# Performance work log

Measured on AMD Instinct MI355X. Metric: run time of the kernel, lower is better.

## Reference

```python
import jax, jax.numpy as jnp
import numpy as np

IOU_THR = 0.5
NEG_POS = 3
CONF_W = 1.0
LOC_W = 1.0


def setup_inputs() -> dict:
    key = jax.random.key(0)
    ks = jax.random.split(key, 6)
    B, A, G = 16, 65536, 32
    ac = jax.random.uniform(ks[0], (B, A, 2))
    asz = jax.random.uniform(ks[1], (B, A, 2)) * 0.28 + 0.02
    anchors = jnp.concatenate([ac - asz / 2, ac + asz / 2], -1)
    gc = jax.random.uniform(ks[2], (B, G, 2))
    gsz = jax.random.uniform(ks[3], (B, G, 2)) * 0.28 + 0.02
    gt_boxes = jnp.concatenate([gc - gsz / 2, gc + gsz / 2], -1)
    bbox_pred = anchors + 0.05 * jax.random.normal(ks[4], (B, A, 4))
    # probabilities strictly inside (0,1) for BCE
    conf_pred = jax.random.uniform(ks[5], (B, A)) * 0.98 + 0.01
    return {"bbox_pred": bbox_pred, "conf_pred": conf_pred,
            "anchors": anchors, "gt_boxes": gt_boxes}


def _box_iou(a, g):
    # a: [A,4] xyxy, g: [G,4] xyxy -> [A,G]
    lt = jnp.maximum(a[:, None, :2], g[None, :, :2])
    rb = jnp.minimum(a[:, None, 2:], g[None, :, 2:])
    wh = jnp.clip(rb - lt, 0.0)
    inter = wh[..., 0] * wh[..., 1]
    area_a = (a[:, 2] - a[:, 0]) * (a[:, 3] - a[:, 1])
    area_g = (g[:, 2] - g[:, 0]) * (g[:, 3] - g[:, 1])
    return inter / (area_a[:, None] + area_g[None, :] - inter)


def _bce(p, t):
    return -(t * jnp.log(p) + (1.0 - t) * jnp.log1p(-p))


def _smooth_l1(x):
    ax = jnp.abs(x)
    return jnp.where(ax < 1.0, 0.5 * ax * ax, ax - 0.5)


def _per_image(bp, cp, an, gt):
    # bp: [A,4] pred boxes, cp: [A] conf, an: [A,4] anchors, gt: [G,4]
    A = cp.shape[0]
    ious = _box_iou(an, gt)                      # [A,G]
    best_gt_iou = ious.max(1)                    # [A]
    best_gt_idx = ious.argmax(1)                 # [A]
    best_anchor_idx = ious.argmax(0)             # [G] force-match each gt
    mask = (best_gt_iou > IOU_THR).at[best_anchor_idx].set(True)
    num_pos = mask.sum()

    # localization loss (center/size parameterization), summed over positives
    matched = gt[best_gt_idx]                    # [A,4]
    pc = (bp[:, :2] + bp[:, 2:]) / 2
    ps = bp[:, 2:] - bp[:, :2]
    gc = (matched[:, :2] + matched[:, 2:]) / 2
    gs = matched[:, 2:] - matched[:, :2]
    loc = _smooth_l1(jnp.concatenate([pc, ps], 1) - jnp.concatenate([gc, gs], 1)).sum(1)
    loc_loss = jnp.where(mask, loc, 0.0).sum()

    # confidence loss with hard negative mining
    t = mask.astype(cp.dtype)
    bce = _bce(cp, t)
    pos_loss = jnp.where(mask, bce, 0.0).sum()
    neg_bce = jnp.where(mask, 0.0, bce)
    num_neg = jnp.minimum(num_pos * NEG_POS, A - num_pos)
    sorted_neg = -jnp.sort(-neg_bce)             # descending
    neg_loss = jnp.where(jnp.arange(A) < num_neg, sorted_neg, 0.0).sum()
    conf_loss = pos_loss / jnp.maximum(num_pos, 1) + neg_loss / jnp.maximum(num_neg, 1)
    return loc_loss, conf_loss, num_pos


def reference(bbox_pred, conf_pred, anchors, gt_boxes):
    loc, conf, npos = jax.vmap(_per_image)(bbox_pred, conf_pred, anchors, gt_boxes)
    B = bbox_pred.shape[0]
    total_npos = jnp.maximum(npos.sum(), 1)
    total_loc = loc.sum() / total_npos * LOC_W
    total_conf = conf.sum() / B * CONF_W
    return total_loc + total_conf
```

## Files before the change

### kernel.cpp

```cpp
#include <hip/hip_runtime.h>

#define BB 16
#define AA 65536
#define GG 32
#define NB 8192
#define KOFF 59904u
#define MBLK (AA / 256)
#define NSEG 16
#define SEGA (AA / NSEG)

__device__ unsigned char      g_mask[(size_t)BB * AA];
__device__ unsigned char      g_bidx[(size_t)BB * AA];
__device__ unsigned long long g_fpart[(size_t)BB * GG * MBLK];
__device__ unsigned int       g_hpart[(size_t)BB * NSEG * (NB/2)];
__device__ float g_spart[BB * NSEG * 2];
__device__ int   g_npart[BB * NSEG];
__device__ float g_loc[BB], g_pos[BB], g_neg[BB];
__device__ int   g_npos[BB], g_nneg[BB];

__device__ __forceinline__ float iou_f(float ax0, float ay0, float ax1, float ay1,
                                       float gx0, float gy0, float gx1, float gy1) {
    float lx = fmaxf(ax0, gx0), ly = fmaxf(ay0, gy0);
    float rx = fminf(ax1, gx1), ry = fminf(ay1, gy1);
    float w = fmaxf(rx - lx, 0.0f), h = fmaxf(ry - ly, 0.0f);
    float inter = w * h;
    float areaa = (ax1 - ax0) * (ay1 - ay0);
    float areag = (gx1 - gx0) * (gy1 - gy0);
    return inter / (areaa + areag - inter);
}

__device__ __forceinline__ float midval(int bin) {
    return __uint_as_float((((unsigned int)bin + KOFF) << 14) | 8192u);
}

__global__ void k_matchforce(const float4* __restrict__ anchors,
                             const float4* __restrict__ gts) {
    __shared__ float4 sg[GG];
    __shared__ unsigned long long wkey[4][GG];
    const int b = blockIdx.y;
    const int t = threadIdx.x;
    if (t < GG) sg[t] = gts[(size_t)b * GG + t];
    __syncthreads();
    const int a = blockIdx.x * 256 + t;
    const int wave = t >> 6, lane = t & 63;
    const float4 av = anchors[(size_t)b * AA + a];
    float best = -1.0f;
    int bg = 0;
#pragma unroll
    for (int g = 0; g < GG; ++g) {
        const float4 gb = sg[g];
        const float v = iou_f(av.x, av.y, av.z, av.w, gb.x, gb.y, gb.z, gb.w);
        if (v > best) { best = v; bg = g; }
        float m = v;
#pragma unroll
        for (int off = 1; off < 64; off <<= 1) m = fmaxf(m, __shfl_xor(m, off, 64));
        const unsigned long long bal = __ballot(v == m);
        const int first = __ffsll((unsigned long long)bal) - 1;
        if (lane == 0) {
            const unsigned int wa = (unsigned int)(blockIdx.x * 256 + wave * 64 + first);
            wkey[wave][g] = ((unsigned long long)__float_as_uint(m) << 32) |
                            (unsigned long long)(0xFFFFFFFFu - wa);
        }
    }
    g_mask[(size_t)b * AA + a] = (best > 0.5f) ? 1 : 0;
    g_bidx[(size_t)b * AA + a] = (unsigned char)bg;
    __syncthreads();
    if (t < GG) {
        unsigned long long k0 = wkey[0][t];
#pragma unroll
        for (int w = 1; w < 4; ++w) { unsigned long long k1 = wkey[w][t]; if (k1 > k0) k0 = k1; }
        g_fpart[((size_t)b * GG + t) * MBLK + blockIdx.x] = k0;
    }
}

__global__ void k_redforce() {
    const int g = blockIdx.x, b = blockIdx.y, t = threadIdx.x;
    __shared__ unsigned long long red[256];
    red[t] = g_fpart[((size_t)b * GG + g) * MBLK + t];
    __syncthreads();
    for (int w = 128; w > 0; w >>= 1) {
        if (t < w) { if (red[t + w] > red[t]) red[t] = red[t + w]; }
        __syncthreads();
    }
    if (t == 0) {
        const unsigned int a = 0xFFFFFFFFu - (unsigned int)(red[0] & 0xFFFFFFFFull);
        g_mask[(size_t)b * AA + a] = 1;
    }
}

__global__ void k_stats(const float4* __restrict__ bbox,
                        const float* __restrict__ conf,
                        const float4* __restrict__ gts) {
    __shared__ float4 sg[GG];
    __shared__ unsigned int hp[NB / 2];
    __shared__ float rf[256], rf2[256];
    __shared__ unsigned int ru[256];
    const int b = blockIdx.y, seg = blockIdx.x, t = threadIdx.x;
    if (t < GG) sg[t] = gts[(size_t)b * GG + t];
    for (int j = t; j < NB / 2; j += 256) hp[j] = 0u;
    __syncthreads();

    const size_t base = (size_t)b * AA + (size_t)seg * SEGA;
    const float4* c4 = (const float4*)(conf + base);
    const uchar4* m4 = (const uchar4*)(g_mask + base);
    const uchar4* x4 = (const uchar4*)(g_bidx + base);
    const float4* bb4 = bbox + base;

    float pos = 0.0f, loc = 0.0f;
    int np = 0;
#pragma unroll
    for (int j = 0; j < SEGA / 1024; ++j) {
        const int idx = j * 256 + t;
        const float4 p4 = c4[idx];
        const uchar4 mm = m4[idx];
        const uchar4 xx = x4[idx];
        const float pv[4] = {p4.x, p4.y, p4.z, p4.w};
        const unsigned char mv[4] = {mm.x, mm.y, mm.z, mm.w};
        const unsigned char xv[4] = {xx.x, xx.y, xx.z, xx.w};
#pragma unroll
        for (int c = 0; c < 4; ++c) {
            const float p = pv[c];
            if (mv[c]) {
                np += 1;
                pos += -logf(p);
                const float4 bv = bb4[4 * idx + c];
                const float4 gb = sg[xv[c]];
                const float d0 = (bv.x + bv.z) * 0.5f - (gb.x + gb.z) * 0.5f;
                const float d1 = (bv.y + bv.w) * 0.5f - (gb.y + gb.w) * 0.5f;
                const float d2 = (bv.z - bv.x) - (gb.z - gb.x);
                const float d3 = (bv.w - bv.y) - (gb.w - gb.y);
                float ds[4] = {d0, d1, d2, d3};
#pragma unroll
                for (int q = 0; q < 4; ++q) {
                    float ax = fabsf(ds[q]);
                    loc += (ax < 1.0f) ? 0.5f * ax * ax : ax - 0.5f;
                }
            } else {
                const float nb = -log1pf(-p);
                int key = (int)(__float_as_uint(nb) >> 14) - (int)KOFF;
                key = key < 0 ? 0 : (key > NB - 1 ? NB - 1 : key);
                atomicAdd(&hp[key >> 1], 1u << ((key & 1) << 4));
            }
        }
    }
    ru[t] = (unsigned int)np; rf[t] = pos; rf2[t] = loc;
    __syncthreads();
    for (int w = 128; w > 0; w >>= 1) {
        if (t < w) { ru[t] += ru[t + w]; rf[t] += rf[t + w]; rf2[t] += rf2[t + w]; }
        __syncthreads();
    }
    if (t == 0) {
        g_npart[b * NSEG + seg] = (int)ru[0];
        g_spart[(b * NSEG + seg) * 2 + 0] = rf[0];
        g_spart[(b * NSEG + seg) * 2 + 1] = rf2[0];
    }
    unsigned int* outp = g_hpart + ((size_t)b * NSEG + seg) * (NB / 2);
    for (int j = t; j < NB / 2; j += 256) outp[j] = hp[j];
}

__global__ void __launch_bounds__(1024) k_select() {
    __shared__ unsigned int hist[NB];
    __shared__ unsigned int ru[1024];
    __shared__ unsigned int s2[32];
    __shared__ float sh_pos, sh_loc;
    __shared__ int sh_np, sh_k, sh_bsel;
    __shared__ unsigned int sh_take;
    __shared__ float rf[1024];

    const int b = blockIdx.x, t = threadIdx.x;
    for (int w = t; w < NB / 2; w += 1024) {
        unsigned int lo = 0, hi = 0;
#pragma unroll
        for (int s = 0; s < NSEG; ++s) {
            const unsigned int v = g_hpart[((size_t)b * NSEG + s) * (NB / 2) + w];
            lo += v & 0xFFFFu; hi += v >> 16;
        }
        hist[2 * w] = lo; hist[2 * w + 1] = hi;
    }
    if (t == 0) {
        int np = 0; float pos = 0.0f, loc = 0.0f;
        for (int s = 0; s < NSEG; ++s) {
            np += g_npart[b * NSEG + s];
            pos += g_spart[(b * NSEG + s) * 2 + 0];
            loc += g_spart[(b * NSEG + s) * 2 + 1];
        }
        sh_np = np; sh_pos = pos; sh_loc = loc;
    }
    __syncthreads();
    const int np_tot = sh_np;

    unsigned int c = 0;
    const int hi = NB - 1 - t * 8;
#pragma unroll
    for (int j = 0; j < 8; ++j) c += hist[hi - j];
    ru[t] = c;
    __syncthreads();
    if (t < 32) {
        unsigned int x = 0;
#pragma unroll
        for (int j = 0; j < 32; ++j) x += ru[t * 32 + j];
        s2[t] = x;
    }
    __syncthreads();
    if (t == 0) {
        int k = 3 * np_tot;
        const int maxneg = AA - np_tot;
        if (k > maxneg) k = maxneg;
        sh_k = k;
        int bsel = NB;
        unsigned int take = 0;
        if (k > 0) {
            unsigned int cum = 0;
            int u = 0;
            while (u < 31 && cum + s2[u] < (unsigned int)k) { cum += s2[u]; ++u; }
            int cc = u * 32;
            while (cc < 1023 && cum + ru[cc] < (unsigned int)k) { cum += ru[cc]; ++cc; }
            const int h2 = NB - 1 - cc * 8;
            int j = 0;
            while (j < 7 && cum + hist[h2 - j] < (unsigned int)k) { cum += hist[h2 - j]; ++j; }
            bsel = h2 - j;
            take = (unsigned int)k - cum;
        }
        sh_bsel = bsel; sh_take = take;
    }
    __syncthreads();
    const int bsel = sh_bsel;
    float negp = 0.0f;
    for (int j = t; j < NB; j += 1024)
        if (j > bsel) { unsigned int cnt = hist[j]; if (cnt) negp += (float)cnt * midval(j); }
    rf[t] = negp;
    __syncthreads();
    for (int w = 512; w > 0; w >>= 1) {
        if (t < w) rf[t] += rf[t + w];
        __syncthreads();
    }
    if (t == 0) {
        float neg = 0.0f;
        if (sh_k > 0) neg = rf[0] + (float)sh_take * midval(bsel < NB ? bsel : 0);
        g_loc[b] = sh_loc; g_pos[b] = sh_pos; g_neg[b] = neg;
        g_npos[b] = np_tot; g_nneg[b] = sh_k;
    }
}

__global__ void k_final(unsigned int* __restrict__ out) {
    if (threadIdx.x == 0) {
        float loc = 0.0f, conf = 0.0f;
        int tot = 0;
        for (int b = 0; b < BB; ++b) {
            loc += g_loc[b];
            const int np = g_npos[b], nn = g_nneg[b];
            conf += g_pos[b] / (float)(np > 1 ? np : 1) +
                    g_neg[b] / (float)(nn > 1 ? nn : 1);
            tot += np;
        }
        const float total = loc / (float)(tot > 1 ? tot : 1) + conf / (float)BB;
        unsigned int u = __float_as_uint(total);
        unsigned int r = 0x7FFFu + ((u >> 16) & 1u);
        unsigned int bf = (u + r) >> 16;
        out[0] = (bf << 16) | bf;
    }
}

extern "C" void kernel_launch(void* const* d_in, const int* in_sizes, int n_in,
                              void* d_out, int out_size, void* d_ws, size_t ws_size,
                              hipStream_t stream) {
    const float4* bbox    = (const float4*)d_in[0];
    const float*  conf    = (const float*)d_in[1];
    const float4* anchors = (const float4*)d_in[2];
    const float4* gts     = (const float4*)d_in[3];

    k_matchforce<<<dim3(MBLK, BB), 256, 0, stream>>>(anchors, gts);
    k_redforce<<<dim3(GG, BB), 256, 0, stream>>>();
    k_stats<<<dim3(NSEG, BB), 256, 0, stream>>>(bbox, conf, gts);
    k_select<<<BB, 1024, 0, stream>>>();
    k_final<<<1, 64, 0, stream>>>((unsigned int*)d_out);
}
```

Measured before the change: 153.9 us.

## Restructure anchor-GT matching: multi-anchor per thread, ratio metric, LDS atomic argmax

Each thread now handles four anchors and keeps a per-GT running best in registers, replacing the per-GT wave shuffle reduction with shared-memory atomicMax/atomicMin over value and index. IoU is replaced by inter/(areaA+areaG), using a fast reciprocal, and the threshold becomes 1/3, which is equivalent to IoU > 0.5. The second-stage reduction shrinks to one 64-lane wave shuffle because there are fewer partial blocks. This aims to cut shuffle and division cost in the matching kernel, at the cost of more registers and approximate reciprocal precision that may change tie-breaking or argmax choices.

Result: no change. 153.1 us (-0.5%).

```diff
diff --git a/kernel.cpp b/kernel.cpp
--- a/kernel.cpp
+++ b/kernel.cpp
@@ -5,7 +5,9 @@
 #define GG 32
 #define NB 8192
 #define KOFF 59904u
-#define MBLK (AA / 256)
+#define AT 4
+#define APB (256 * AT)
+#define MBLK (AA / APB)
 #define NSEG 16
 #define SEGA (AA / NSEG)
 
@@ -18,72 +20,96 @@
 __device__ float g_loc[BB], g_pos[BB], g_neg[BB];
 __device__ int   g_npos[BB], g_nneg[BB];
 
-__device__ __forceinline__ float iou_f(float ax0, float ay0, float ax1, float ay1,
-                                       float gx0, float gy0, float gx1, float gy1) {
-    float lx = fmaxf(ax0, gx0), ly = fmaxf(ay0, gy0);
-    float rx = fminf(ax1, gx1), ry = fminf(ay1, gy1);
-    float w = fmaxf(rx - lx, 0.0f), h = fmaxf(ry - ly, 0.0f);
-    float inter = w * h;
-    float areaa = (ax1 - ax0) * (ay1 - ay0);
-    float areag = (gx1 - gx0) * (gy1 - gy0);
-    return inter / (areaa + areag - inter);
-}
-
 __device__ __forceinline__ float midval(int bin) {
     return __uint_as_float((((unsigned int)bin + KOFF) << 14) | 8192u);
 }
 
-__global__ void k_matchforce(const float4* __restrict__ anchors,
-                             const float4* __restrict__ gts) {
+__global__ void __launch_bounds__(256, 3)
+k_matchforce(const float4* __restrict__ anchors,
+             const float4* __restrict__ gts) {
     __shared__ float4 sg[GG];
-    __shared__ unsigned long long wkey[4][GG];
+    __shared__ float sga[GG];
+    __shared__ unsigned int vmax[GG];
+    __shared__ unsigned int amin[GG];
     const int b = blockIdx.y;
     const int t = threadIdx.x;
-    if (t < GG) sg[t] = gts[(size_t)b * GG + t];
-    __syncthreads();
-    const int a = blockIdx.x * 256 + t;
-    const int wave = t >> 6, lane = t & 63;
-    const float4 av = anchors[(size_t)b * AA + a];
-    float best = -1.0f;
-    int bg = 0;
+    if (t < GG) {
+        const float4 g4 = gts[(size_t)b * GG + t];
+        sg[t] = g4;
+        sga[t] = (g4.z - g4.x) * (g4.w - g4.y);
+        vmax[t] = 0u;
+        amin[t] = 0xFFFFFFFFu;
+    }
+    __syncthreads();
+
+    const size_t abase = (size_t)b * AA + (size_t)blockIdx.x * APB;
+
+    float ax0[AT], ay0[AT], ax1[AT], ay1[AT], aar[AT], best[AT];
+    int bg[AT];
+#pragma unroll
+    for (int j = 0; j < AT; ++j) {
+        const float4 av = anchors[abase + j * 256 + t];
+        ax0[j] = av.x; ay0[j] = av.y; ax1[j] = av.z; ay1[j] = av.w;
+        aar[j] = (av.z - av.x) * (av.w - av.y);
+        best[j] = -1.0f; bg[j] = 0;
+    }
+    float fl[GG]; int fid[GG];
+#pragma unroll
+    for (int g = 0; g < GG; ++g) { fl[g] = 0.0f; fid[g] = t; }
+
 #pragma unroll
     for (int g = 0; g < GG; ++g) {
         const float4 gb = sg[g];
-        const float v = iou_f(av.x, av.y, av.z, av.w, gb.x, gb.y, gb.z, gb.w);
-        if (v > best) { best = v; bg = g; }
-        float m = v;
-#pragma unroll
-        for (int off = 1; off < 64; off <<= 1) m = fmaxf(m, __shfl_xor(m, off, 64));
-        const unsigned long long bal = __ballot(v == m);
-        const int first = __ffsll((unsigned long long)bal) - 1;
-        if (lane == 0) {
-            const unsigned int wa = (unsigned int)(blockIdx.x * 256 + wave * 64 + first);
-            wkey[wave][g] = ((unsigned long long)__float_as_uint(m) << 32) |
-                            (unsigned long long)(0xFFFFFFFFu - wa);
-        }
-    }
-    g_mask[(size_t)b * AA + a] = (best > 0.5f) ? 1 : 0;
-    g_bidx[(size_t)b * AA + a] = (unsigned char)bg;
+        const float ga = sga[g];
+#pragma unroll
+        for (int j = 0; j < AT; ++j) {
+            const float lx = fmaxf(ax0[j], gb.x), ly = fmaxf(ay0[j], gb.y);
+            const float rx = fminf(ax1[j], gb.z), ry = fminf(ay1[j], gb.w);
+            const float w = fmaxf(rx - lx, 0.0f), h = fmaxf(ry - ly, 0.0f);
+            const float inter = w * h;
+            const float s = aar[j] + ga;
+            const float r = inter * __builtin_amdgcn_rcpf(s);
+            if (r > best[j]) { best[j] = r; bg[j] = g; }
+            if (r > fl[g])   { fl[g] = r; fid[g] = j * 256 + t; }
+        }
+    }
+
+#pragma unroll
+    for (int j = 0; j < AT; ++j) {
+        g_mask[abase + j * 256 + t] = (best[j] > (1.0f / 3.0f)) ? 1 : 0;
+        g_bidx[abase + j * 256 + t] = (unsigned char)bg[j];
+    }
+
+#pragma unroll
+    for (int g = 0; g < GG; ++g) {
+        if (fl[g] > __uint_as_float(vmax[g]))
+            atomicMax(&vmax[g], __float_as_uint(fl[g]));
+    }
+    __syncthreads();
+#pragma unroll
+    for (int g = 0; g < GG; ++g) {
+        if (__float_as_uint(fl[g]) == vmax[g])
+            atomicMin(&amin[g], (unsigned int)fid[g]);
+    }
     __syncthreads();
     if (t < GG) {
-        unsigned long long k0 = wkey[0][t];
-#pragma unroll
-        for (int w = 1; w < 4; ++w) { unsigned long long k1 = wkey[w][t]; if (k1 > k0) k0 = k1; }
-        g_fpart[((size_t)b * GG + t) * MBLK + blockIdx.x] = k0;
+        const unsigned int ga = (unsigned int)(blockIdx.x * APB) + amin[t];
+        g_fpart[((size_t)b * GG + t) * MBLK + blockIdx.x] =
+            ((unsigned long long)vmax[t] << 32) |
+            (unsigned long long)(0xFFFFFFFFu - ga);
     }
 }
 
 __global__ void k_redforce() {
     const int g = blockIdx.x, b = blockIdx.y, t = threadIdx.x;
-    __shared__ unsigned long long red[256];
-    red[t] = g_fpart[((size_t)b * GG + g) * MBLK + t];
-    __syncthreads();
-    for (int w = 128; w > 0; w >>= 1) {
-        if (t < w) { if (red[t + w] > red[t]) red[t] = red[t + w]; }
-        __syncthreads();
-    }
-    if (t == 0) {
-        const unsigned int a = 0xFFFFFFFFu - (unsigned int)(red[0] & 0xFFFFFFFFull);
+    unsigned long long k = g_fpart[((size_t)b * GG + g) * MBLK + t];
+#pragma unroll
+    for (int off = 32; off > 0; off >>= 1) {
+        const unsigned long long o = __shfl_xor(k, off, 64);
+        if (o > k) k = o;
+    }
+    if (t == 0) {
+        const unsigned int a = 0xFFFFFFFFu - (unsigned int)(k & 0xFFFFFFFFull);
         g_mask[(size_t)b * AA + a] = 1;
     }
 }
@@ -270,7 +296,7 @@
     const float4* gts     = (const float4*)d_in[3];
 
     k_matchforce<<<dim3(MBLK, BB), 256, 0, stream>>>(anchors, gts);
-    k_redforce<<<dim3(GG, BB), 256, 0, stream>>>();
+    k_redforce<<<dim3(GG, BB), 64, 0, stream>>>();
     k_stats<<<dim3(NSEG, BB), 256, 0, stream>>>(bbox, conf, gts);
     k_select<<<BB, 1024, 0, stream>>>();
     k_final<<<1, 64, 0, stream>>>((unsigned int*)d_out);
```
